# Optimization experiments

Measured on AMD Instinct MI355X. Metric: run time of the kernel, lower is better.

## Reference

```python
import jax, jax.numpy as jnp
import numpy as np

B, N, C, DIN, DOUT = 16, 65536, 256, 16, 16  # ratio = N // C = 256 nodes per cluster


def setup_inputs() -> dict:
    key = jax.random.key(0)
    k1, k2, k3, k4, k5 = jax.random.split(key, 5)
    stdv = 1.0 / np.sqrt(DOUT)
    x = jax.random.normal(k1, (B, N, DIN), dtype=jnp.float32)
    # parameters, pre-reshaped: torch w_diag (in*out, C) with out-major io axis -> (out, in, C)
    w_diag = jax.random.uniform(k2, (DOUT, DIN, C), jnp.float32, -stdv, stdv)
    w_off = jax.random.uniform(k3, (DOUT, DIN, C, C), jnp.float32, -stdv, stdv)
    b1 = jax.random.uniform(k4, (DOUT,), jnp.float32, -stdv, stdv)
    # flatten_ids(cluster_ids): a permutation putting each cluster's nodes contiguous
    permute_ids = jax.random.permutation(k5, N)
    return {"x": x, "w_diag": w_diag, "w_off": w_off, "b1": b1, "permute_ids": permute_ids}


def reference(x, w_diag, w_off, b1, permute_ids):
    # Faithful to: W = rearrange(kron(diag_embed(w_diag), I_r)) + (1/N) rearrange(kron(w_off, 1_{rxr}))
    # out = inv_permute( reshape( W @ flatten(permute(x)) ) ) + b1,
    # computed via the block-constant structure instead of materializing the (Dout*N, Din*N) W.
    Bq, Nn, Din = x.shape
    Dout, _, Cc = w_diag.shape
    ratio = Nn // Cc
    inv_permute = jnp.argsort(permute_ids)
    xp = x[:, permute_ids, :]                       # (B, N, Din), cluster-contiguous
    xc = xp.reshape(Bq, Cc, ratio, Din)             # (B, C, r, Din)
    # diagonal blocks: per-cluster Din->Dout mixing, identity over within-cluster index
    out_diag = jnp.einsum('oic,bcri->bcro', w_diag, xc)   # (B, C, r, Dout)
    # off blocks: constant within each (cluster j, cluster k) block -> use cluster sums
    s = xc.sum(axis=2)                              # (B, C, Din)
    out_off = jnp.einsum('oick,bki->bco', w_off, s) / Nn  # (B, C, Dout)
    out = out_diag + out_off[:, :, None, :]         # broadcast over within-cluster index
    out = out.reshape(Bq, Nn, Dout)[:, inv_permute, :] + b1[None, None, :]
    return out
```

## Files before the change

kernel.cpp:

```cpp
#include <hip/hip_runtime.h>

#define B_    16
#define N_    65536
#define C_    256
#define DIN_  16
#define DOUT_ 16


__global__ __launch_bounds__(256) void k_sum_prep(
    const float* __restrict__ x, const float* __restrict__ w_diag,
    const int* __restrict__ P, float* __restrict__ s,
    float* __restrict__ wd_t, int* __restrict__ c_of_n)
{
    int bid = blockIdx.x;
    int t = threadIdx.x;
    if (bid >= B_ * C_) {
        int r = bid - B_ * C_;
        if (r < 256) {
            int o = r >> 4, i = r & 15;
            wd_t[t * 256 + i * 16 + o] = w_diag[r * C_ + t];
        } else {
            int k = r - 256;
            c_of_n[P[k * 256 + t]] = k;
        }
        return;
    }
    int b = bid >> 8;
    int k = bid & (C_ - 1);
    int q  = t & 3;
    int rg = t >> 2;
    float4 acc = make_float4(0.f, 0.f, 0.f, 0.f);
    const int jbase = k << 8;
    #pragma unroll
    for (int m = 0; m < 4; ++m) {
        int n = P[jbase + rg + 64 * m];
        const float4* row =
            reinterpret_cast<const float4*>(x + ((size_t)(b * N_ + n)) * DIN_);
        float4 v = row[q];
        acc.x += v.x; acc.y += v.y; acc.z += v.z; acc.w += v.w;
    }
    #pragma unroll
    for (int mask = 4; mask <= 32; mask <<= 1) {
        acc.x += __shfl_xor(acc.x, mask, 64);
        acc.y += __shfl_xor(acc.y, mask, 64);
        acc.z += __shfl_xor(acc.z, mask, 64);
        acc.w += __shfl_xor(acc.w, mask, 64);
    }
    __shared__ float4 part[4][4];
    int lane = t & 63, wave = t >> 6;
    if (lane < 4) part[wave][lane] = acc;
    __syncthreads();
    if (t < 16) {
        int qq = t >> 2, comp = t & 3;
        float v = 0.f;
        #pragma unroll
        for (int w = 0; w < 4; ++w) {
            const float* p = reinterpret_cast<const float*>(&part[w][qq]);
            v += p[comp];
        }
        int i = qq * 4 + comp;
        s[i * (B_ * C_) + b * C_ + k] = v;
    }
}

__global__ __launch_bounds__(512) void k_off(
    const float* __restrict__ w_off, const float* __restrict__ s,
    const float* __restrict__ b1, float* __restrict__ off)
{
    const int c  = (int)blockIdx.x >> 1;
    const int og = (int)blockIdx.x & 1;
    const int t  = threadIdx.x;
    const int kq = t & 63;
    const int w  = t >> 6;
    const int oq = w & 1;
    const int bh = w >> 1;
    const int b0 = bh * 4;
    const int o0 = og * 8 + oq * 4;

    __shared__ float4 slds[2][1024];

    const float4* s4 = reinterpret_cast<const float4*>(s);
    const float4* w4 = reinterpret_cast<const float4*>(w_off);

    int wbase[4];
    #pragma unroll
    for (int o4 = 0; o4 < 4; ++o4)
        wbase[o4] = (o0 + o4) * 262144 + c * 64 + kq;

    float acc[16];
    #pragma unroll
    for (int z = 0; z < 16; ++z) acc[z] = 0.f;

    float4 wA[4], wB[4], sA[2], sB[2];

    {
        float4 p0 = s4[t], p1 = s4[t + 512];
        #pragma unroll
        for (int o4 = 0; o4 < 4; ++o4) wA[o4] = w4[wbase[o4]];
        sA[0] = s4[1024 + t];
        sA[1] = s4[1024 + t + 512];
        slds[0][t] = p0;
        slds[0][t + 512] = p1;
        asm volatile("s_waitcnt lgkmcnt(0)" ::: "memory");
        __builtin_amdgcn_s_barrier();
    }

#define K2_BODY(I, WC, WN, SR, SI, RB)                                         \
    {                                                                          \
        if ((I) + 2 < DIN_) {                                                  \
            SI[0] = s4[((I) + 2) * 1024 + t];                                  \
            SI[1] = s4[((I) + 2) * 1024 + t + 512];                            \
        }                                                                      \
        if ((I) + 1 < DIN_) {                                                  \
            _Pragma("unroll")                                                  \
            for (int o4 = 0; o4 < 4; ++o4)                                     \
                WN[o4] = w4[wbase[o4] + ((I) + 1) * 16384];                    \
        }                                                                      \
        _Pragma("unroll")                                                      \
        for (int bq = 0; bq < 4; ++bq) {                                       \
            float4 sv = slds[RB][(b0 + bq) * 64 + kq];                         \
            _Pragma("unroll")                                                  \
            for (int o4 = 0; o4 < 4; ++o4)                                     \
                acc[o4 * 4 + bq] += WC[o4].x * sv.x + WC[o4].y * sv.y          \
                                  + WC[o4].z * sv.z + WC[o4].w * sv.w;         \
        }                                                                      \
        if ((I) + 1 < DIN_) {                                                  \
            slds[(RB) ^ 1][t]       = SR[0];                                   \
            slds[(RB) ^ 1][t + 512] = SR[1];                                   \
            asm volatile("s_waitcnt lgkmcnt(0)" ::: "memory");                 \
            __builtin_amdgcn_s_barrier();                                      \
        }                                                                      \
    }

    #pragma unroll
    for (int ih = 0; ih < DIN_ / 2; ++ih) {
        K2_BODY(2 * ih,     wA, wB, sA, sB, 0)
        K2_BODY(2 * ih + 1, wB, wA, sB, sA, 1)
    }
#undef K2_BODY

#define FOLD(MASK, CNT)                                                        \
    {                                                                          \
        const bool hi_ = (kq & (MASK)) != 0;                                   \
        _Pragma("unroll")                                                      \
        for (int j = 0; j < (CNT); ++j) {                                      \
            float keep = hi_ ? acc[j + (CNT)] : acc[j];                        \
            float send = hi_ ? acc[j] : acc[j + (CNT)];                        \
            acc[j] = keep + __shfl_xor(send, (MASK), 64);                      \
        }                                                                      \
    }
    FOLD(1, 8) FOLD(2, 4) FOLD(4, 2) FOLD(8, 1)
#undef FOLD
    acc[0] += __shfl_xor(acc[0], 16, 64);
    acc[0] += __shfl_xor(acc[0], 32, 64);

    if (kq < 16) {
        int j  = ((kq & 1) << 3) | ((kq & 2) << 1) | ((kq & 4) >> 1) | ((kq & 8) >> 3);
        int b  = b0 + (j & 3);
        int o  = o0 + (j >> 2);
        off[((b << 8) + c) * DOUT_ + o] = acc[0] * (1.0f / (float)N_) + b1[o];
    }
}

__global__ __launch_bounds__(256) void k_apply_seq(
    const float* __restrict__ x, const int* __restrict__ c_of_n,
    const float* __restrict__ wd_t, const float* __restrict__ off,
    float* __restrict__ out)
{
    int t = threadIdx.x;
    int lr = t >> 2, q = t & 3;
    int n = blockIdx.x * 64 + lr;
    int c = c_of_n[n];

    const float4* wd4 = reinterpret_cast<const float4*>(wd_t);
    float4 wds[16];
    #pragma unroll
    for (int i = 0; i < 16; ++i) wds[i] = wd4[c * 64 + i * 4 + q];

    const float4* x4   = reinterpret_cast<const float4*>(x);
    const float4* off4 = reinterpret_cast<const float4*>(off);
    float4* out4       = reinterpret_cast<float4*>(out);

    #pragma unroll 2
    for (int b = 0; b < B_; ++b) {
        size_t rowbase = ((size_t)(b * N_ + n)) * 4;
        float4 x0 = x4[rowbase + 0];
        float4 x1 = x4[rowbase + 1];
        float4 x2 = x4[rowbase + 2];
        float4 x3 = x4[rowbase + 3];
        float4 acc = off4[((size_t)((b << 8) + c)) * 4 + q];
        float xv[16];
        xv[0]=x0.x; xv[1]=x0.y; xv[2]=x0.z; xv[3]=x0.w;
        xv[4]=x1.x; xv[5]=x1.y; xv[6]=x1.z; xv[7]=x1.w;
        xv[8]=x2.x; xv[9]=x2.y; xv[10]=x2.z; xv[11]=x2.w;
        xv[12]=x3.x; xv[13]=x3.y; xv[14]=x3.z; xv[15]=x3.w;
        #pragma unroll
        for (int i = 0; i < 16; ++i) {
            acc.x += xv[i] * wds[i].x;
            acc.y += xv[i] * wds[i].y;
            acc.z += xv[i] * wds[i].z;
            acc.w += xv[i] * wds[i].w;
        }
        out4[rowbase + q] = acc;
    }
}

extern "C" void kernel_launch(void* const* d_in, const int* in_sizes, int n_in,
                              void* d_out, int out_size, void* d_ws, size_t ws_size,
                              hipStream_t stream) {
    const float* x      = (const float*)d_in[0];
    const float* w_diag = (const float*)d_in[1];
    const float* w_off  = (const float*)d_in[2];
    const float* b1     = (const float*)d_in[3];
    const int*   P      = (const int*)d_in[4];
    float* out    = (float*)d_out;
    float* s      = (float*)d_ws;
    float* off    = s + 65536;
    float* wd_t   = off + 65536;
    int*   c_of_n = (int*)(wd_t + 65536);

    k_sum_prep<<<B_ * C_ + 512, 256, 0, stream>>>(x, w_diag, P, s, wd_t, c_of_n);
    k_off<<<C_ * 2, 512, 0, stream>>>(w_off, s, b1, off);
    k_apply_seq<<<N_ / 64, 256, 0, stream>>>(x, c_of_n, wd_t, off, out);
}
```

Before: 208.3 us.

## Replace gathered cluster sums with coalesced LDS-atomic scatter, split k_off finer

```diff
diff --git a/kernel.cpp b/kernel.cpp
--- a/kernel.cpp
+++ b/kernel.cpp
@@ -6,76 +6,76 @@
 #define DIN_  16
 #define DOUT_ 16
 
-
-__global__ __launch_bounds__(256) void k_sum_prep(
-    const float* __restrict__ x, const float* __restrict__ w_diag,
-    const int* __restrict__ P, float* __restrict__ s,
-    float* __restrict__ wd_t, int* __restrict__ c_of_n)
+typedef float f32x4 __attribute__((ext_vector_type(4)));
+
+
+__global__ __launch_bounds__(256) void k_pre(
+    const int* __restrict__ P, float* __restrict__ s, int* __restrict__ c_of_n)
 {
     int bid = blockIdx.x;
     int t = threadIdx.x;
-    if (bid >= B_ * C_) {
-        int r = bid - B_ * C_;
-        if (r < 256) {
-            int o = r >> 4, i = r & 15;
-            wd_t[t * 256 + i * 16 + o] = w_diag[r * C_ + t];
-        } else {
-            int k = r - 256;
-            c_of_n[P[k * 256 + t]] = k;
-        }
+    if (bid < 64) {
+        reinterpret_cast<float4*>(s)[bid * 256 + t] =
+            make_float4(0.f, 0.f, 0.f, 0.f);
+    } else {
+        int k = bid - 64;
+        c_of_n[P[k * 256 + t]] = k;
+    }
+}
+
+__global__ __launch_bounds__(256) void k_scat(
+    const float* __restrict__ x, const float* __restrict__ w_diag,
+    const int* __restrict__ c_of_n, float* __restrict__ s,
+    float* __restrict__ wd_t)
+{
+    int bid = blockIdx.x;
+    int t = threadIdx.x;
+    if (bid >= 512) {
+        int r = bid - 512;
+        int o = r >> 4, i = r & 15;
+        wd_t[t * 256 + i * 16 + o] = w_diag[r * C_ + t];
         return;
     }
-    int b = bid >> 8;
-    int k = bid & (C_ - 1);
-    int q  = t & 3;
-    int rg = t >> 2;
-    float4 acc = make_float4(0.f, 0.f, 0.f, 0.f);
-    const int jbase = k << 8;
-    #pragma unroll
-    for (int m = 0; m < 4; ++m) {
-        int n = P[jbase + rg + 64 * m];
-        const float4* row =
-            reinterpret_cast<const float4*>(x + ((size_t)(b * N_ + n)) * DIN_);
-        float4 v = row[q];
-        acc.x += v.x; acc.y += v.y; acc.z += v.z; acc.w += v.w;
-    }
-    #pragma unroll
-    for (int mask = 4; mask <= 32; mask <<= 1) {
-        acc.x += __shfl_xor(acc.x, mask, 64);
-        acc.y += __shfl_xor(acc.y, mask, 64);
-        acc.z += __shfl_xor(acc.z, mask, 64);
-        acc.w += __shfl_xor(acc.w, mask, 64);
-    }
-    __shared__ float4 part[4][4];
-    int lane = t & 63, wave = t >> 6;
-    if (lane < 4) part[wave][lane] = acc;
+    __shared__ float s_loc[256 * 17];
+    #pragma unroll
+    for (int r = t; r < 256 * 17; r += 256) s_loc[r] = 0.f;
     __syncthreads();
-    if (t < 16) {
-        int qq = t >> 2, comp = t & 3;
-        float v = 0.f;
-        #pragma unroll
-        for (int w = 0; w < 4; ++w) {
-            const float* p = reinterpret_cast<const float*>(&part[w][qq]);
-            v += p[comp];
-        }
-        int i = qq * 4 + comp;
-        s[i * (B_ * C_) + b * C_ + k] = v;
-    }
-}
-
-__global__ __launch_bounds__(512) void k_off(
+
+    int b    = bid >> 5;
+    int ch   = bid & 31;
+    int n0   = ch * 2048;
+    int quad = t & 3;
+    int rsub = t >> 2;
+
+    const float4* x4 = reinterpret_cast<const float4*>(x);
+    const size_t base = ((size_t)b * N_ + n0) * 4;
+
+    for (int it = 0; it < 32; ++it) {
+        int nl = it * 64 + rsub;
+        int k  = c_of_n[n0 + nl];
+        float4 v = x4[base + (size_t)nl * 4 + quad];
+        float* dst = &s_loc[k * 17 + quad * 4];
+        atomicAdd(dst + 0, v.x);
+        atomicAdd(dst + 1, v.y);
+        atomicAdd(dst + 2, v.z);
+        atomicAdd(dst + 3, v.w);
+    }
+    __syncthreads();
+    #pragma unroll
+    for (int i = 0; i < 16; ++i)
+        atomicAdd(&s[i * 4096 + b * 256 + t], s_loc[t * 17 + i]);
+}
+
+__global__ __launch_bounds__(512, 6) void k_off(
     const float* __restrict__ w_off, const float* __restrict__ s,
     const float* __restrict__ b1, float* __restrict__ off)
 {
-    const int c  = (int)blockIdx.x >> 1;
-    const int og = (int)blockIdx.x & 1;
+    const int c  = (int)blockIdx.x >> 2;
+    const int o0 = ((int)blockIdx.x & 3) * 4;
     const int t  = threadIdx.x;
     const int kq = t & 63;
     const int w  = t >> 6;
-    const int oq = w & 1;
-    const int bh = w >> 1;
-    const int b0 = bh * 4;
-    const int o0 = og * 8 + oq * 4;
+    const int b0 = w * 2;
 
     __shared__ float4 slds[2][1024];
 
@@ -87,9 +87,9 @@
     for (int o4 = 0; o4 < 4; ++o4)
         wbase[o4] = (o0 + o4) * 262144 + c * 64 + kq;
 
-    float acc[16];
-    #pragma unroll
-    for (int z = 0; z < 16; ++z) acc[z] = 0.f;
+    float acc[8];
+    #pragma unroll
+    for (int z = 0; z < 8; ++z) acc[z] = 0.f;
 
     float4 wA[4], wB[4], sA[2], sB[2];
 
@@ -117,11 +117,11 @@
                 WN[o4] = w4[wbase[o4] + ((I) + 1) * 16384];                    \
         }                                                                      \
         _Pragma("unroll")                                                      \
-        for (int bq = 0; bq < 4; ++bq) {                                       \
+        for (int bq = 0; bq < 2; ++bq) {                                       \
             float4 sv = slds[RB][(b0 + bq) * 64 + kq];                         \
             _Pragma("unroll")                                                  \
             for (int o4 = 0; o4 < 4; ++o4)                                     \
-                acc[o4 * 4 + bq] += WC[o4].x * sv.x + WC[o4].y * sv.y          \
+                acc[o4 * 2 + bq] += WC[o4].x * sv.x + WC[o4].y * sv.y          \
                                   + WC[o4].z * sv.z + WC[o4].w * sv.w;         \
         }                                                                      \
         if ((I) + 1 < DIN_) {                                                  \
@@ -149,15 +149,18 @@
             acc[j] = keep + __shfl_xor(send, (MASK), 64);                      \
         }                                                                      \
     }
-    FOLD(1, 8) FOLD(2, 4) FOLD(4, 2) FOLD(8, 1)
+    FOLD(1, 4) FOLD(2, 2) FOLD(4, 1)
 #undef FOLD
+    acc[0] += __shfl_xor(acc[0], 8, 64);
     acc[0] += __shfl_xor(acc[0], 16, 64);
     acc[0] += __shfl_xor(acc[0], 32, 64);
 
-    if (kq < 16) {
-        int j  = ((kq & 1) << 3) | ((kq & 2) << 1) | ((kq & 4) >> 1) | ((kq & 8) >> 3);
-        int b  = b0 + (j & 3);
-        int o  = o0 + (j >> 2);
+    if (kq < 8) {
+        int j  = ((kq & 1) << 2) | (kq & 2) | ((kq & 4) >> 2);
+        int bq = j & 1;
+        int o4 = j >> 1;
+        int b  = b0 + bq;
+        int o  = o0 + o4;
         off[((b << 8) + c) * DOUT_ + o] = acc[0] * (1.0f / (float)N_) + b1[o];
     }
 }
@@ -179,7 +182,7 @@
 
     const float4* x4   = reinterpret_cast<const float4*>(x);
     const float4* off4 = reinterpret_cast<const float4*>(off);
-    float4* out4       = reinterpret_cast<float4*>(out);
+    f32x4* out4        = reinterpret_cast<f32x4*>(out);
 
     #pragma unroll 2
     for (int b = 0; b < B_; ++b) {
@@ -201,7 +204,9 @@
             acc.z += xv[i] * wds[i].z;
             acc.w += xv[i] * wds[i].w;
         }
-        out4[rowbase + q] = acc;
+        f32x4 accv;
+        accv.x = acc.x; accv.y = acc.y; accv.z = acc.z; accv.w = acc.w;
+        __builtin_nontemporal_store(accv, &out4[rowbase + q]);
     }
 }
 
@@ -219,7 +224,8 @@
     float* wd_t   = off + 65536;
     int*   c_of_n = (int*)(wd_t + 65536);
 
-    k_sum_prep<<<B_ * C_ + 512, 256, 0, stream>>>(x, w_diag, P, s, wd_t, c_of_n);
-    k_off<<<C_ * 2, 512, 0, stream>>>(w_off, s, b1, off);
+    k_pre<<<320, 256, 0, stream>>>(P, s, c_of_n);
+    k_scat<<<768, 256, 0, stream>>>(x, w_diag, c_of_n, s, wd_t);
+    k_off<<<C_ * 4, 512, 0, stream>>>(w_off, s, b1, off);
     k_apply_seq<<<N_ / 64, 256, 0, stream>>>(x, c_of_n, wd_t, off, out);
 }
```

After: 292.1 us. 1.4x slower.

## Restructure off-block matvec to drop LDS staging and use nontemporal output stores

Applied to the files above, without the earlier changes.

```diff
diff --git a/kernel.cpp b/kernel.cpp
--- a/kernel.cpp
+++ b/kernel.cpp
@@ -5,6 +5,8 @@
 #define C_    256
 #define DIN_  16
 #define DOUT_ 16
+
+typedef float f32x4 __attribute__((ext_vector_type(4)));
 
 
 __global__ __launch_bounds__(256) void k_sum_prep(
@@ -59,85 +61,44 @@
             v += p[comp];
         }
         int i = qq * 4 + comp;
-        s[i * (B_ * C_) + b * C_ + k] = v;
+        s[(b * DIN_ + i) * C_ + k] = v;
     }
 }
 
-__global__ __launch_bounds__(512) void k_off(
+__global__ __launch_bounds__(512, 4) void k_off(
     const float* __restrict__ w_off, const float* __restrict__ s,
     const float* __restrict__ b1, float* __restrict__ off)
 {
-    const int c  = (int)blockIdx.x >> 1;
-    const int og = (int)blockIdx.x & 1;
+    const int g  = (int)blockIdx.x;
+    const int c  = g & 255;
+    const int b0 = (g >> 8) * 8;
     const int t  = threadIdx.x;
     const int kq = t & 63;
-    const int w  = t >> 6;
-    const int oq = w & 1;
-    const int bh = w >> 1;
-    const int b0 = bh * 4;
-    const int o0 = og * 8 + oq * 4;
+    const int wv = t >> 6;
+    const int o0 = wv * 2;
 
-    __shared__ float4 slds[2][1024];
+    const float4* w4 = reinterpret_cast<const float4*>(w_off);
+    const float4* s4 = reinterpret_cast<const float4*>(s);
 
-    const float4* s4 = reinterpret_cast<const float4*>(s);
-    const float4* w4 = reinterpret_cast<const float4*>(w_off);
-
-    int wbase[4];
-    #pragma unroll
-    for (int o4 = 0; o4 < 4; ++o4)
-        wbase[o4] = (o0 + o4) * 262144 + c * 64 + kq;
+    const int wb0 = ((o0 * 16) * 256 + c) * 64 + kq;
+    const int wb1 = wb0 + 262144;
+    const int sb  = (b0 * 16) * 64 + kq;
 
     float acc[16];
     #pragma unroll
     for (int z = 0; z < 16; ++z) acc[z] = 0.f;
 
-    float4 wA[4], wB[4], sA[2], sB[2];
-
-    {
-        float4 p0 = s4[t], p1 = s4[t + 512];
+    #pragma unroll
+    for (int i = 0; i < DIN_; ++i) {
+        float4 w0 = w4[wb0 + i * 16384];
+        float4 w1 = w4[wb1 + i * 16384];
         #pragma unroll
-        for (int o4 = 0; o4 < 4; ++o4) wA[o4] = w4[wbase[o4]];
-        sA[0] = s4[1024 + t];
-        sA[1] = s4[1024 + t + 512];
-        slds[0][t] = p0;
-        slds[0][t + 512] = p1;
-        asm volatile("s_waitcnt lgkmcnt(0)" ::: "memory");
-        __builtin_amdgcn_s_barrier();
+        for (int bb = 0; bb < 8; ++bb) {
+            float4 sv = s4[sb + (bb * 16 + i) * 64];
+            acc[bb]     += w0.x * sv.x + w0.y * sv.y + w0.z * sv.z + w0.w * sv.w;
+            acc[8 + bb] += w1.x * sv.x + w1.y * sv.y + w1.z * sv.z + w1.w * sv.w;
+        }
     }
-
-#define K2_BODY(I, WC, WN, SR, SI, RB)                                         \
-    {                                                                          \
-        if ((I) + 2 < DIN_) {                                                  \
-            SI[0] = s4[((I) + 2) * 1024 + t];                                  \
-            SI[1] = s4[((I) + 2) * 1024 + t + 512];                            \
-        }                                                                      \
-        if ((I) + 1 < DIN_) {                                                  \
-            _Pragma("unroll")                                                  \
-            for (int o4 = 0; o4 < 4; ++o4)                                     \
-                WN[o4] = w4[wbase[o4] + ((I) + 1) * 16384];                    \
-        }                                                                      \
-        _Pragma("unroll")                                                      \
-        for (int bq = 0; bq < 4; ++bq) {                                       \
-            float4 sv = slds[RB][(b0 + bq) * 64 + kq];                         \
-            _Pragma("unroll")                                                  \
-            for (int o4 = 0; o4 < 4; ++o4)                                     \
-                acc[o4 * 4 + bq] += WC[o4].x * sv.x + WC[o4].y * sv.y          \
-                                  + WC[o4].z * sv.z + WC[o4].w * sv.w;         \
-        }                                                                      \
-        if ((I) + 1 < DIN_) {                                                  \
-            slds[(RB) ^ 1][t]       = SR[0];                                   \
-            slds[(RB) ^ 1][t + 512] = SR[1];                                   \
-            asm volatile("s_waitcnt lgkmcnt(0)" ::: "memory");                 \
-            __builtin_amdgcn_s_barrier();                                      \
-        }                                                                      \
-    }
-
-    #pragma unroll
-    for (int ih = 0; ih < DIN_ / 2; ++ih) {
-        K2_BODY(2 * ih,     wA, wB, sA, sB, 0)
-        K2_BODY(2 * ih + 1, wB, wA, sB, sA, 1)
-    }
-#undef K2_BODY
 
 #define FOLD(MASK, CNT)                                                        \
     {                                                                          \
@@ -156,8 +117,10 @@
 
     if (kq < 16) {
         int j  = ((kq & 1) << 3) | ((kq & 2) << 1) | ((kq & 4) >> 1) | ((kq & 8) >> 3);
-        int b  = b0 + (j & 3);
-        int o  = o0 + (j >> 2);
+        int oo = j >> 3;
+        int bb = j & 7;
+        int b  = b0 + bb;
+        int o  = o0 + oo;
         off[((b << 8) + c) * DOUT_ + o] = acc[0] * (1.0f / (float)N_) + b1[o];
     }
 }
@@ -179,7 +142,7 @@
 
     const float4* x4   = reinterpret_cast<const float4*>(x);
     const float4* off4 = reinterpret_cast<const float4*>(off);
-    float4* out4       = reinterpret_cast<float4*>(out);
+    f32x4* out4        = reinterpret_cast<f32x4*>(out);
 
     #pragma unroll 2
     for (int b = 0; b < B_; ++b) {
@@ -201,7 +164,9 @@
             acc.z += xv[i] * wds[i].z;
             acc.w += xv[i] * wds[i].w;
         }
-        out4[rowbase + q] = acc;
+        f32x4 accv;
+        accv.x = acc.x; accv.y = acc.y; accv.z = acc.z; accv.w = acc.w;
+        __builtin_nontemporal_store(accv, &out4[rowbase + q]);
     }
 }
 
@@ -220,6 +185,6 @@
     int*   c_of_n = (int*)(wd_t + 65536);
 
     k_sum_prep<<<B_ * C_ + 512, 256, 0, stream>>>(x, w_diag, P, s, wd_t, c_of_n);
-    k_off<<<C_ * 2, 512, 0, stream>>>(w_off, s, b1, off);
+    k_off<<<512, 512, 0, stream>>>(w_off, s, b1, off);
     k_apply_seq<<<N_ / 64, 256, 0, stream>>>(x, c_of_n, wd_t, off, out);
 }
```

After: 214.5 us. +3.0%, slower.
